# Kernel tuning notes

Hardware: AMD Instinct MI355X
Metric: run time of the kernel (lower is better)

The kernel has to match this reference:

```python
import jax, jax.numpy as jnp
import numpy as np

PAD = 1
VOCAB, D, HOPS = 32000, 256, 3

def _gru_dir(x_tbd, h0, Wih, Whh, bih, bhh):
    # x_tbd: [T,B,D]; PyTorch GRU gate math
    def step(h, xt):
        gx = xt @ Wih.T + bih            # [B,3D]
        gh = h @ Whh.T + bhh
        xr, xz, xn = jnp.split(gx, 3, axis=-1)
        hr, hz, hn = jnp.split(gh, 3, axis=-1)
        r = jax.nn.sigmoid(xr + hr)
        z = jax.nn.sigmoid(xz + hz)
        n = jnp.tanh(xn + r * hn)
        h2 = (1.0 - z) * n + z * h
        return h2, h2
    hT, ys = jax.lax.scan(step, h0, x_tbd)
    return ys, hT

def _embed_bag(table, idx):
    # idx: [B,L,M] -> sum over M -> [B,L,D]
    return jnp.take(table, idx, axis=0).sum(axis=2)

def _add_lm(full_mem, kb_len, conv_len, hiddens):
    # full_mem: [B,L,D]; hiddens: [B,T,D]; write hiddens into rows [kb, kb+cl)
    B, L, _ = full_mem.shape
    T = hiddens.shape[1]
    pos = jnp.arange(L)[None, :]                      # [1,L]
    rel = pos - kb_len[:, None]                        # [B,L]
    valid = (rel >= 0) & (rel < conv_len[:, None])
    rel_c = jnp.clip(rel, 0, T - 1)
    gathered = jnp.take_along_axis(hiddens, rel_c[:, :, None], axis=1)  # [B,L,D]
    return full_mem + jnp.where(valid[:, :, None], gathered, 0.0)

def setup_inputs() -> dict:
    key = jax.random.key(0)
    ks = jax.random.split(key, 20)
    B, T, L, M = 32, 128, 512, 4
    conv_seqs = jax.random.randint(ks[0], (B, T, M), 0, VOCAB)
    src_seqs = jax.random.randint(ks[1], (B, L, M), 0, VOCAB)
    kb_len = jnp.full((B,), L - T, dtype=jnp.int32)
    conv_len = jnp.full((B,), T, dtype=jnp.int32)
    def zero_pad(t):
        return t.at[PAD].set(0.0)
    emb_ctx = zero_pad(0.1 * jax.random.normal(ks[2], (VOCAB, D)))
    C_tables = zero_pad(0.1 * jax.random.normal(ks[3], (HOPS + 1, VOCAB, D)).transpose(1, 0, 2)).transpose(1, 0, 2)
    s = 1.0 / np.sqrt(D)
    Wih_f = jax.random.uniform(ks[4], (3 * D, D), minval=-s, maxval=s)
    Whh_f = jax.random.uniform(ks[5], (3 * D, D), minval=-s, maxval=s)
    bih_f = jax.random.uniform(ks[6], (3 * D,), minval=-s, maxval=s)
    bhh_f = jax.random.uniform(ks[7], (3 * D,), minval=-s, maxval=s)
    Wih_b = jax.random.uniform(ks[8], (3 * D, D), minval=-s, maxval=s)
    Whh_b = jax.random.uniform(ks[9], (3 * D, D), minval=-s, maxval=s)
    bih_b = jax.random.uniform(ks[10], (3 * D,), minval=-s, maxval=s)
    bhh_b = jax.random.uniform(ks[11], (3 * D,), minval=-s, maxval=s)
    W_w = jax.random.uniform(ks[12], (D, 2 * D), minval=-s, maxval=s)
    W_b = jax.random.uniform(ks[13], (D,), minval=-s, maxval=s)
    proj_w = jax.random.uniform(ks[14], (D, 2 * D), minval=-s, maxval=s)
    proj_b = jax.random.uniform(ks[15], (D,), minval=-s, maxval=s)
    return dict(conv_seqs=conv_seqs, src_seqs=src_seqs, kb_len=kb_len, conv_len=conv_len,
                emb_ctx=emb_ctx, C_tables=C_tables,
                Wih_f=Wih_f, Whh_f=Whh_f, bih_f=bih_f, bhh_f=bhh_f,
                Wih_b=Wih_b, Whh_b=Whh_b, bih_b=bih_b, bhh_b=bhh_b,
                W_w=W_w, W_b=W_b, proj_w=proj_w, proj_b=proj_b)

def reference(conv_seqs, src_seqs, kb_len, conv_len, emb_ctx, C_tables,
              Wih_f, Whh_f, bih_f, bhh_f, Wih_b, Whh_b, bih_b, bhh_b,
              W_w, W_b, proj_w, proj_b):
    B = conv_seqs.shape[0]
    # ContextRNN (dropout is identity at eval)
    emb = _embed_bag(emb_ctx, conv_seqs)               # [B,T,D]
    x = emb.transpose(1, 0, 2)                          # [T,B,D]
    h0 = jnp.zeros((B, D), emb.dtype)
    ys_f, hT_f = _gru_dir(x, h0, Wih_f, Whh_f, bih_f, bhh_f)
    ys_b, hT_b = _gru_dir(x[::-1], h0, Wih_b, Whh_b, bih_b, bhh_b)
    outputs = jnp.concatenate([ys_f, ys_b[::-1]], axis=-1).transpose(1, 0, 2)  # [B,T,2D]
    hidden = jnp.concatenate([hT_f, hT_b], axis=-1) @ W_w.T + W_b              # [B,D]
    rnn_out = outputs @ W_w.T + W_b                                            # [B,T,D]
    # ExternalKnowledge encode
    u = hidden
    prob_logit = None
    embed_C = None
    for hop in range(HOPS):
        embed_A = _add_lm(_embed_bag(C_tables[hop], src_seqs), kb_len, conv_len, rnn_out)
        embed_C = _add_lm(_embed_bag(C_tables[hop + 1], src_seqs), kb_len, conv_len, rnn_out)
        prob_logit = jnp.einsum('bld,bd->bl', embed_A, u)
        prob = jax.nn.softmax(prob_logit, axis=1)
        o_k = jnp.einsum('bld,bl->bd', embed_C, prob)
        u = u + o_k
    global_pointer = jax.nn.sigmoid(prob_logit)
    encoded = jax.nn.relu(jnp.concatenate([hidden, u], axis=-1) @ proj_w.T + proj_b)[None]
    return global_pointer, encoded
```

## Files before the change

kernel.cpp:

```cpp
#include <hip/hip_runtime.h>

typedef _Float16 f16;
typedef _Float16 f16x8 __attribute__((ext_vector_type(8)));
typedef _Float16 f16x4 __attribute__((ext_vector_type(4)));
typedef float    f32x4 __attribute__((ext_vector_type(4)));


__device__ __forceinline__ float frcp(float x){
  float r; asm("v_rcp_f32 %0, %1" : "=v"(r) : "v"(x)); return r;
}
__device__ __forceinline__ float fsig(float x){ return frcp(1.0f + __expf(-x)); }
__device__ __forceinline__ float ftanh(float x){ return 2.0f*frcp(1.0f + __expf(-2.0f*x)) - 1.0f; }

__global__ void k_zero(float* out){
  int i = blockIdx.x*256 + threadIdx.x;
  if (i < 24576) out[i] = 0.f;
}

__global__ __launch_bounds__(256) void k_prep(const float* __restrict__ s0,
                                              const float* __restrict__ s1,
                                              const float* __restrict__ s2,
                                              const float* __restrict__ s3,
                                              const float* __restrict__ s4,
                                              f16* __restrict__ d0, f16* __restrict__ d1,
                                              f16* __restrict__ d2, f16* __restrict__ d3,
                                              f16* __restrict__ d4,
                                              const int* __restrict__ conv,
                                              const float* __restrict__ tbl,
                                              f16* __restrict__ emb){
  int bid = blockIdx.x;
  if (bid < 768){
    int i = bid*256 + threadIdx.x;
    d0[i] = (f16)s0[i];
    d1[i] = (f16)s1[i];
    d2[i] = (f16)s2[i];
    d3[i] = (f16)s3[i];
    if (i < 131072) d4[i] = (f16)s4[i];
    return;
  }
  int bt = bid - 768, d = threadIdx.x;
  const int* ix = conv + (size_t)bt*4;
  float s = 0.f;
#pragma unroll
  for (int m = 0; m < 4; ++m) s += tbl[(size_t)ix[m]*256 + d];
  emb[(size_t)bt*256 + d] = (f16)s;
}

__global__ __launch_bounds__(256) void k_gx2(const f16* __restrict__ emb,
                                             const f16* __restrict__ wf,
                                             const f16* __restrict__ wb,
                                             const float* __restrict__ bih_f,
                                             const float* __restrict__ bhh_f,
                                             const float* __restrict__ bih_b,
                                             const float* __restrict__ bhh_b,
                                             f16* __restrict__ gx_f,
                                             f16* __restrict__ gx_b){
  int rev = blockIdx.x >> 6, blk = blockIdx.x & 63;
  const f16* W16 = rev ? wb : wf;
  const float* bih = rev ? bih_b : bih_f;
  const float* bhh = rev ? bhh_b : bhh_f;
  f16* gx = rev ? gx_b : gx_f;

  int lane = threadIdx.x & 63, wv = threadIdx.x >> 6;
  int l16 = lane & 15, l4 = lane >> 4;
  int mrow = blk*64 + wv*16;
  int m = mrow + l16;
  int t = m >> 5, b = m & 31;
  int tsrc = rev ? (127 - t) : t;
  const f16* arow = emb + (size_t)(b*128 + tsrc)*256;
  f16x8 af[8];
#pragma unroll
  for (int kt = 0; kt < 8; ++kt) af[kt] = *(const f16x8*)(arow + kt*32 + l4*8);

  for (int nt = 0; nt < 48; ++nt){
    int n = nt*16 + l16;
    const f16* brow = W16 + (size_t)n*256;
    f32x4 acc = {0.f,0.f,0.f,0.f};
#pragma unroll
    for (int kt = 0; kt < 8; ++kt){
      f16x8 bf = *(const f16x8*)(brow + kt*32 + l4*8);
      acc = __builtin_amdgcn_mfma_f32_16x16x32_f16(af[kt], bf, acc, 0, 0, 0);
    }
    float bias = bih[n] + (n < 512 ? bhh[n] : 0.f);
#pragma unroll
    for (int r = 0; r < 4; ++r){
      int m2 = mrow + l4*4 + r;
      gx[(size_t)m2*768 + n] = (f16)(acc[r] + bias);
    }
  }
}

__global__ __launch_bounds__(512, 1) void k_grumega(const f16* __restrict__ gx_f,
                                                    const f16* __restrict__ gx_b,
                                                    const f16* __restrict__ whhf16,
                                                    const f16* __restrict__ whhb16,
                                                    const float* __restrict__ bhh_f,
                                                    const float* __restrict__ bhh_b,
                                                    f16* __restrict__ Abuf,
                                                    const int* __restrict__ src,
                                                    const float* __restrict__ Ct,
                                                    f16* __restrict__ bagT,
                                                    int tab0, int tab1, int tab2, int tab3){
  int bid = blockIdx.x;
  if (bid >= 4){
    int gi = bid - 4;
    int slot = gi >> 6;
    int tab = slot == 0 ? tab0 : slot == 1 ? tab1 : slot == 2 ? tab2 : tab3;
    const float* tbl = Ct + (size_t)tab * 32000 * 256;
    f16* dst = bagT + (size_t)slot * 4194304;
    int tid = threadIdx.x;
    int d = tid & 255, half = tid >> 8;
    int base = (gi & 63) * 256;
#pragma unroll 2
    for (int it = 0; it < 128; ++it){
      int task = base + it*2 + half;
      int4 ix = *(const int4*)(src + (size_t)task*4);
      float s = tbl[(size_t)ix.x*256 + d] + tbl[(size_t)ix.y*256 + d]
              + tbl[(size_t)ix.z*256 + d] + tbl[(size_t)ix.w*256 + d];
      dst[(size_t)task*256 + d] = (f16)s;
    }
    return;
  }

  int dir = bid >> 1, grp = bid & 1, b0 = grp*16;
  const f16*   gx  = dir ? gx_b   : gx_f;
  const f16*   Whh = dir ? whhb16 : whhf16;
  const float* bhh = dir ? bhh_b  : bhh_f;

  int tid = threadIdx.x, lane = tid & 63, wv = tid >> 6;
  int l16 = lane & 15, l4 = lane >> 4;

  __shared__ __align__(16) f16   a16[2][16][264];
  __shared__ __align__(16) float bhnL[256];
  for (int i = tid; i < (16*264*2)/4; i += 512) ((unsigned*)&a16[0][0][0])[i] = 0u;
  if (tid < 256) bhnL[tid] = bhh[512 + tid];

  f16x8 aW[2][3][8];
#pragma unroll
  for (int q = 0; q < 2; ++q){
    int Q = 2*wv + q;
#pragma unroll
    for (int g = 0; g < 3; ++g){
      const f16* wrow = Whh + (size_t)(g*256 + Q*16 + l16)*256;
#pragma unroll
      for (int kt = 0; kt < 8; ++kt) aW[q][g][kt] = *(const f16x8*)(wrow + kt*32 + l4*8);
    }
  }

  const f16* gp = gx + (size_t)(b0 + l16)*768;
  f16* ap  = Abuf + (size_t)(b0 + l16)*128*512 + dir*256 + (size_t)(dir ? 127 : 0)*512;
  int  astep = dir ? -512 : 512;
  f16* app = ap;

  const int d00 = (2*wv    )*16 + l4*4;
  const int d01 = (2*wv + 1)*16 + l4*4;

  f16x4 pend[2];
  pend[0] = (f16x4){(f16)0.f,(f16)0.f,(f16)0.f,(f16)0.f};
  pend[1] = (f16x4){(f16)0.f,(f16)0.f,(f16)0.f,(f16)0.f};

  __syncthreads();

#pragma unroll 1
  for (int t = 0; t < 128; ++t){
    if (t){
      *(f16x4*)(app + d00) = pend[0];
      *(f16x4*)(app + d01) = pend[1];
    }
    f16x4 xg[2][3];
#pragma unroll
    for (int q = 0; q < 2; ++q)
#pragma unroll
      for (int g = 0; g < 3; ++g)
        xg[q][g] = *(const f16x4*)(gp + g*256 + (2*wv+q)*16 + l4*4);

    const f16* rb = &a16[t & 1][l16][l4*8];

    f32x4 accr[2], accz[2];
#pragma unroll
    for (int q = 0; q < 2; ++q){ accr[q] = (f32x4){0.f,0.f,0.f,0.f};
                                 accz[q] = (f32x4){0.f,0.f,0.f,0.f}; }
#pragma unroll
    for (int kt = 0; kt < 8; ++kt){
      f16x8 bf = *(const f16x8*)(rb + kt*32);
#pragma unroll
      for (int q = 0; q < 2; ++q){
        accr[q] = __builtin_amdgcn_mfma_f32_16x16x32_f16(aW[q][0][kt], bf, accr[q], 0, 0, 0);
        accz[q] = __builtin_amdgcn_mfma_f32_16x16x32_f16(aW[q][1][kt], bf, accz[q], 0, 0, 0);
      }
    }
    f32x4 accn[2];
#pragma unroll
    for (int q = 0; q < 2; ++q) accn[q] = (f32x4){0.f,0.f,0.f,0.f};
#pragma unroll
    for (int kt = 0; kt < 8; ++kt){
      f16x8 bf = *(const f16x8*)(rb + kt*32);
#pragma unroll
      for (int q = 0; q < 2; ++q)
        accn[q] = __builtin_amdgcn_mfma_f32_16x16x32_f16(aW[q][2][kt], bf, accn[q], 0, 0, 0);
    }
    float rr[2][4], zz[2][4];
#pragma unroll
    for (int q = 0; q < 2; ++q)
#pragma unroll
      for (int r = 0; r < 4; ++r){
        rr[q][r] = fsig((float)xg[q][0][r] + accr[q][r]);
        zz[q][r] = fsig((float)xg[q][1][r] + accz[q][r]);
      }
    int nxt = (t & 1) ^ 1;
#pragma unroll
    for (int q = 0; q < 2; ++q){
      int d0 = (2*wv+q)*16 + l4*4;
      float4 bh4 = *(const float4*)(&bhnL[d0]);
      f16x4 hold = pend[q];
      f16x4 o4;
#pragma unroll
      for (int r = 0; r < 4; ++r){
        float bh = (r==0)?bh4.x:(r==1)?bh4.y:(r==2)?bh4.z:bh4.w;
        float nn = ftanh((float)xg[q][2][r] + rr[q][r]*(accn[q][r] + bh));
        float h2 = nn + zz[q][r]*((float)hold[r] - nn);
        o4[r] = (f16)h2;
      }
      *(f16x4*)(&a16[nxt][l16][d0]) = o4;
      pend[q] = o4;
    }
    app = ap; ap += astep;
    gp += 24576;
    __syncthreads();
  }
  *(f16x4*)(app + d00) = pend[0];
  *(f16x4*)(app + d01) = pend[1];
}

__global__ __launch_bounds__(256) void k_post(const f16* __restrict__ Abuf,
                                              const f16* __restrict__ Ww16,
                                              const float* __restrict__ Wb,
                                              float* __restrict__ rnn,
                                              float* __restrict__ hidden,
                                              float* __restrict__ u){
  int bid = blockIdx.x;
  int lane = threadIdx.x & 63, wv = threadIdx.x >> 6;
  int l16 = lane & 15, l4 = lane >> 4;
  if (bid < 64){
    int mrow = bid*64 + wv*16;
    const f16* arow = Abuf + (size_t)(mrow + l16)*512;
    f16x8 af[16];
#pragma unroll
    for (int kt = 0; kt < 16; ++kt) af[kt] = *(const f16x8*)(arow + kt*32 + l4*8);
    for (int nt = 0; nt < 16; ++nt){
      int n = nt*16 + l16;
      const f16* brow = Ww16 + (size_t)n*512;
      f32x4 acc = {0.f,0.f,0.f,0.f};
#pragma unroll
      for (int kt = 0; kt < 16; ++kt){
        f16x8 bf = *(const f16x8*)(brow + kt*32 + l4*8);
        acc = __builtin_amdgcn_mfma_f32_16x16x32_f16(af[kt], bf, acc, 0, 0, 0);
      }
      float bias = Wb[n];
#pragma unroll
      for (int r = 0; r < 4; ++r)
        rnn[(size_t)(mrow + l4*4 + r)*256 + n] = acc[r] + bias;
    }
    return;
  }
  int hb = bid - 64;
  int mt = wv & 1, nt = hb*2 + (wv >> 1);
  int b = mt*16 + l16;
  const f16* rowf = Abuf + ((size_t)b*128 + 127)*512;
  const f16* rowb = Abuf + ((size_t)b*128)*512;
  f16x8 af[16];
#pragma unroll
  for (int kt = 0; kt < 16; ++kt){
    int k = kt*32 + l4*8;
    af[kt] = *(const f16x8*)((k < 256 ? rowf : rowb) + k);
  }
  int n = nt*16 + l16;
  const f16* brow = Ww16 + (size_t)n*512;
  f32x4 acc = {0.f,0.f,0.f,0.f};
#pragma unroll
  for (int kt = 0; kt < 16; ++kt){
    f16x8 bf = *(const f16x8*)(brow + kt*32 + l4*8);
    acc = __builtin_amdgcn_mfma_f32_16x16x32_f16(af[kt], bf, acc, 0, 0, 0);
  }
  float bias = Wb[n];
#pragma unroll
  for (int r = 0; r < 4; ++r){
    int bo = mt*16 + l4*4 + r;
    float v = acc[r] + bias;
    hidden[(size_t)bo*256 + n] = v;
    u[(size_t)bo*256 + n] = v;
  }
}

__global__ __launch_bounds__(256) void k_logits(const int* __restrict__ src,
                                                const int* __restrict__ kbl,
                                                const int* __restrict__ cvl,
                                                const float* __restrict__ tblA,
                                                const float* __restrict__ rnn,
                                                const float* __restrict__ u,
                                                float* __restrict__ logits,
                                                const f16* __restrict__ bag){
  int b = blockIdx.x >> 5, chunk = blockIdx.x & 31;
  int lane = threadIdx.x & 63, wv = threadIdx.x >> 6;
  int kb = kbl[b], cl = cvl[b];
  float4 uv = *(const float4*)(u + b*256 + lane*4);
#pragma unroll
  for (int i = 0; i < 4; ++i){
    int l = chunk*16 + wv*4 + i;
    float b0, b1, b2, b3;
    if (bag){
      f16x4 bv = *(const f16x4*)(bag + ((size_t)b*512 + l)*256 + lane*4);
      b0 = (float)bv[0]; b1 = (float)bv[1]; b2 = (float)bv[2]; b3 = (float)bv[3];
    } else {
      const int* sp = src + ((size_t)b*512 + l)*4;
      b0 = b1 = b2 = b3 = 0.f;
#pragma unroll
      for (int m = 0; m < 4; ++m){
        float4 wq = *(const float4*)(tblA + (size_t)sp[m]*256 + lane*4);
        b0 += wq.x; b1 += wq.y; b2 += wq.z; b3 += wq.w;
      }
    }
    int rel = l - kb;
    if (rel >= 0 && rel < cl){
      int rc = rel < 127 ? rel : 127;
      float4 rv = *(const float4*)(rnn + ((size_t)b*128 + rc)*256 + lane*4);
      b0 += rv.x; b1 += rv.y; b2 += rv.z; b3 += rv.w;
    }
    float p = b0*uv.x + b1*uv.y + b2*uv.z + b3*uv.w;
#pragma unroll
    for (int off = 32; off >= 1; off >>= 1) p += __shfl_down(p, off);
    if (lane == 0) logits[(size_t)b*512 + l] = p;
  }
}

__global__ __launch_bounds__(256) void k_okv(const int* __restrict__ src,
                                             const int* __restrict__ kbl,
                                             const int* __restrict__ cvl,
                                             const float* __restrict__ tblC,
                                             const float* __restrict__ rnn,
                                             const float* __restrict__ logits,
                                             float* __restrict__ u,
                                             float* __restrict__ gp_out, int write_gp,
                                             const f16* __restrict__ bagin,
                                             f16* __restrict__ bagout){
  int b = blockIdx.x >> 4, c = blockIdx.x & 15;
  int d = threadIdx.x, lane = d & 63, wv = d >> 6;
  __shared__ float red[4];
  __shared__ float bc;
  __shared__ float pr[512];
  __shared__ int   sidx[128];

  float v0 = logits[(size_t)b*512 + d];
  float v1 = logits[(size_t)b*512 + 256 + d];
  float m = fmaxf(v0, v1);
#pragma unroll
  for (int off = 32; off >= 1; off >>= 1) m = fmaxf(m, __shfl_down(m, off));
  if (lane == 0) red[wv] = m;
  __syncthreads();
  if (d == 0) bc = fmaxf(fmaxf(red[0], red[1]), fmaxf(red[2], red[3]));
  __syncthreads();
  float mx = bc;
  float e0 = __expf(v0 - mx), e1 = __expf(v1 - mx);
  float s = e0 + e1;
#pragma unroll
  for (int off = 32; off >= 1; off >>= 1) s += __shfl_down(s, off);
  __syncthreads();
  if (lane == 0) red[wv] = s;
  __syncthreads();
  if (d == 0) bc = red[0] + red[1] + red[2] + red[3];
  __syncthreads();
  float inv = 1.0f/bc;
  pr[d] = e0*inv; pr[256 + d] = e1*inv;
  if (d < 128) sidx[d] = src[(size_t)b*2048 + c*128 + d];
  if (write_gp && c == 0){
    gp_out[(size_t)b*512 + d]       = fsig(v0);
    gp_out[(size_t)b*512 + 256 + d] = fsig(v1);
  }
  __syncthreads();

  int kb = kbl[b], cl = cvl[b];
  float acc = 0.f;
  for (int l = 0; l < 32; ++l){
    float bag;
    if (bagin){
      bag = (float)bagin[((size_t)b*512 + c*32 + l)*256 + d];
    } else {
      const int* sp = sidx + l*4;
      bag = tblC[(size_t)sp[0]*256 + d] + tblC[(size_t)sp[1]*256 + d]
          + tblC[(size_t)sp[2]*256 + d] + tblC[(size_t)sp[3]*256 + d];
      if (bagout) bagout[((size_t)b*512 + c*32 + l)*256 + d] = (f16)bag;
    }
    int rel = (c*32 + l) - kb;
    if (rel >= 0 && rel < cl){
      int rc = rel < 127 ? rel : 127;
      bag += rnn[((size_t)b*128 + rc)*256 + d];
    }
    acc += pr[c*32 + l] * bag;
  }
  atomicAdd(&u[(size_t)b*256 + d], acc);
}

__global__ void k_encoded(const float* __restrict__ hidden, const float* __restrict__ u,
                          const float* __restrict__ pw, const float* __restrict__ pb,
                          float* __restrict__ out){
  int b = blockIdx.x, d = threadIdx.x;
  const float* w = pw + (size_t)d*512;
  float s = pb[d];
  for (int k = 0; k < 256; ++k) s += hidden[b*256 + k] * w[k];
  for (int k = 0; k < 256; ++k) s += u[b*256 + k]      * w[256 + k];
  out[(size_t)b*256 + d] = fmaxf(s, 0.f);
}

extern "C" void kernel_launch(void* const* d_in, const int* in_sizes, int n_in,
                              void* d_out, int out_size, void* d_ws, size_t ws_size,
                              hipStream_t stream){
  (void)in_sizes; (void)n_in; (void)out_size;
  float* out = (float*)d_out;

  const size_t WS_NEEDED = 25034752;
  if (ws_size < WS_NEEDED){
    k_zero<<<96, 256, 0, stream>>>(out);
    return;
  }

  const int* conv  = (const int*)d_in[0];
  const int* src   = (const int*)d_in[1];
  const int* kbl   = (const int*)d_in[2];
  const int* cvl   = (const int*)d_in[3];
  const float* emb_ctx = (const float*)d_in[4];
  const float* Ct      = (const float*)d_in[5];
  const float* Wih_f = (const float*)d_in[6];
  const float* Whh_f = (const float*)d_in[7];
  const float* bih_f = (const float*)d_in[8];
  const float* bhh_f = (const float*)d_in[9];
  const float* Wih_b = (const float*)d_in[10];
  const float* Whh_b = (const float*)d_in[11];
  const float* bih_b = (const float*)d_in[12];
  const float* bhh_b = (const float*)d_in[13];
  const float* Ww = (const float*)d_in[14];
  const float* Wb = (const float*)d_in[15];
  const float* pw = (const float*)d_in[16];
  const float* pb = (const float*)d_in[17];

  char* ws = (char*)d_ws;
  f16*   emb    = (f16*)(ws);
  f16*   gx_f   = (f16*)(ws + 2097152);
  f16*   gx_b   = (f16*)(ws + 8388608);
  f16*   Abuf   = (f16*)(ws + 14680064);
  float* rnn    = (float*)(ws + 18874368);
  float* hidden = (float*)(ws + 23068672);
  float* u      = (float*)(ws + 23101440);
  float* logits = (float*)(ws + 23134208);
  f16*   wihf16 = (f16*)(ws + 23199744);
  f16*   wihb16 = (f16*)(ws + 23592960);
  f16*   whhf16 = (f16*)(ws + 23986176);
  f16*   whhb16 = (f16*)(ws + 24379392);
  f16*   ww16   = (f16*)(ws + 24772608);
  f16*   bagbuf = (f16*)(ws + 2097152);
  f16*   bagT   = (f16*)(ws + WS_NEEDED);
  size_t avail  = ws_size - WS_NEEDED;
  int ntab = (int)(avail / 8388608); if (ntab > 4) ntab = 4;
  const int tabids[4] = {1, 2, 3, 0};
  const f16* bt[4] = {nullptr, nullptr, nullptr, nullptr};
  for (int s = 0; s < ntab; ++s) bt[tabids[s]] = bagT + (size_t)s*4194304;

  k_prep<<<4864, 256, 0, stream>>>(Wih_f, Wih_b, Whh_f, Whh_b, Ww,
                                   wihf16, wihb16, whhf16, whhb16, ww16,
                                   conv, emb_ctx, emb);
  k_gx2<<<128, 256, 0, stream>>>(emb, wihf16, wihb16,
                                 bih_f, bhh_f, bih_b, bhh_b, gx_f, gx_b);
  k_grumega<<<4 + 64*ntab, 512, 0, stream>>>(gx_f, gx_b, whhf16, whhb16,
                                             bhh_f, bhh_b, Abuf,
                                             src, Ct, bagT,
                                             tabids[0], tabids[1], tabids[2], tabids[3]);
  k_post<<<72, 256, 0, stream>>>(Abuf, ww16, Wb, rnn, hidden, u);

  for (int hop = 0; hop < 3; ++hop){
    const float* tA = Ct + (size_t)hop     * 32000 * 256;
    const float* tC = Ct + (size_t)(hop+1) * 32000 * 256;
    const f16* lbag = bt[hop] ? bt[hop] : (hop ? bagbuf : (const f16*)nullptr);
    const f16* obag = bt[hop + 1];
    f16* obout = (!obag && hop < 2) ? bagbuf : (f16*)nullptr;
    k_logits<<<1024, 256, 0, stream>>>(src, kbl, cvl, tA, rnn, u, logits, lbag);
    k_okv<<<512, 256, 0, stream>>>(src, kbl, cvl, tC, rnn, logits, u,
                                   out, hop == 2 ? 1 : 0, obag, obout);
  }
  k_encoded<<<32, 256, 0, stream>>>(hidden, u, pw, pb, out + 16384);
}
```

Measured before the change: 745.3 us.

## Fuse each memory hop into one per-batch kernel when all bags are precomputed

When all four embedding-bag tables are precomputed in workspace, each hop's logits, softmax, weighted sum and u update run in a single 32-block kernel per hop. The last hop also computes the global pointer and the encoded projection, which replaces the separate logits, okv and encoded launches. This removes launch overhead and intermediate logits traffic. The cost is only 32 blocks of parallelism, with per-thread serial 256-element loops, including strided column reads over the C bag.

```diff
diff --git a/kernel.cpp b/kernel.cpp
--- a/kernel.cpp
+++ b/kernel.cpp
@@ -292,6 +292,120 @@
   }
 }
 
+__global__ __launch_bounds__(512) void k_hop(const int* __restrict__ kbl,
+                                             const int* __restrict__ cvl,
+                                             const f16* __restrict__ bagA,
+                                             const f16* __restrict__ bagC,
+                                             const float* __restrict__ rnn,
+                                             float* __restrict__ u,
+                                             float* __restrict__ gp_out, int last,
+                                             const float* __restrict__ hidden,
+                                             const float* __restrict__ pw,
+                                             const float* __restrict__ pb,
+                                             float* __restrict__ enc_out){
+  int b = blockIdx.x, tid = threadIdx.x;
+  int lane = tid & 63, wvi = tid >> 6;
+  __shared__ float uL[256];
+  __shared__ float pr[512];
+  __shared__ float redm[8], reds[8];
+  __shared__ float bcast;
+  __shared__ float part[2][256];
+
+  if (tid < 256) uL[tid] = u[(size_t)b*256 + tid];
+  __syncthreads();
+
+  int kb = kbl[b], cl = cvl[b];
+
+  const f16* brow = bagA + ((size_t)b*512 + tid)*256;
+  int rel = tid - kb;
+  bool inr = (rel >= 0 && rel < cl);
+  int rc = rel < 127 ? rel : 127;
+  const float* rrow = rnn + ((size_t)b*128 + (inr ? rc : 0))*256;
+  float dot = 0.f;
+  if (inr){
+    for (int k = 0; k < 256; k += 8){
+      f16x8 bv = *(const f16x8*)(brow + k);
+      float4 r0 = *(const float4*)(rrow + k);
+      float4 r1 = *(const float4*)(rrow + k + 4);
+      dot += ((float)bv[0]+r0.x)*uL[k+0] + ((float)bv[1]+r0.y)*uL[k+1]
+           + ((float)bv[2]+r0.z)*uL[k+2] + ((float)bv[3]+r0.w)*uL[k+3]
+           + ((float)bv[4]+r1.x)*uL[k+4] + ((float)bv[5]+r1.y)*uL[k+5]
+           + ((float)bv[6]+r1.z)*uL[k+6] + ((float)bv[7]+r1.w)*uL[k+7];
+    }
+  } else {
+    for (int k = 0; k < 256; k += 8){
+      f16x8 bv = *(const f16x8*)(brow + k);
+      dot += (float)bv[0]*uL[k+0] + (float)bv[1]*uL[k+1]
+           + (float)bv[2]*uL[k+2] + (float)bv[3]*uL[k+3]
+           + (float)bv[4]*uL[k+4] + (float)bv[5]*uL[k+5]
+           + (float)bv[6]*uL[k+6] + (float)bv[7]*uL[k+7];
+    }
+  }
+  if (last) gp_out[(size_t)b*512 + tid] = fsig(dot);
+
+  float m = dot;
+#pragma unroll
+  for (int off = 32; off >= 1; off >>= 1) m = fmaxf(m, __shfl_down(m, off));
+  if (lane == 0) redm[wvi] = m;
+  __syncthreads();
+  if (tid == 0){
+    float mm = redm[0];
+#pragma unroll
+    for (int i = 1; i < 8; ++i) mm = fmaxf(mm, redm[i]);
+    bcast = mm;
+  }
+  __syncthreads();
+  float e = __expf(dot - bcast);
+  float s = e;
+#pragma unroll
+  for (int off = 32; off >= 1; off >>= 1) s += __shfl_down(s, off);
+  if (lane == 0) reds[wvi] = s;
+  __syncthreads();
+  float stot = reds[0]+reds[1]+reds[2]+reds[3]+reds[4]+reds[5]+reds[6]+reds[7];
+  pr[tid] = e * frcp(stot);
+  __syncthreads();
+
+  int d = tid & 255, hf = tid >> 8;
+  const f16* cbase = bagC + ((size_t)b*512 + hf*256)*256 + d;
+  const float* rbase = rnn + (size_t)b*128*256 + d;
+  float acc = 0.f;
+  for (int l = 0; l < 256; ++l){
+    int gl = hf*256 + l;
+    float bag = (float)cbase[(size_t)l*256];
+    int r2 = gl - kb;
+    if (r2 >= 0 && r2 < cl){
+      int rc2 = r2 < 127 ? r2 : 127;
+      bag += rbase[(size_t)rc2*256];
+    }
+    acc += pr[gl] * bag;
+  }
+  part[hf][d] = acc;
+  __syncthreads();
+  if (tid < 256){
+    float un = uL[tid] + part[0][tid] + part[1][tid];
+    u[(size_t)b*256 + tid] = un;
+    uL[tid] = un;
+  }
+  __syncthreads();
+
+  if (last){
+    __shared__ float hL[256];
+    if (tid < 256) hL[tid] = hidden[(size_t)b*256 + tid];
+    __syncthreads();
+    const float* w = pw + (size_t)d*512 + hf*256;
+    const float* xv = hf ? uL : hL;
+    float sacc = 0.f;
+    for (int k = 0; k < 256; k += 4){
+      float4 wq = *(const float4*)(w + k);
+      sacc += wq.x*xv[k] + wq.y*xv[k+1] + wq.z*xv[k+2] + wq.w*xv[k+3];
+    }
+    part[hf][d] = sacc;
+    __syncthreads();
+    if (tid < 256)
+      enc_out[(size_t)b*256 + tid] = fmaxf(part[0][tid] + part[1][tid] + pb[tid], 0.f);
+  }
+}
+
 __global__ __launch_bounds__(256) void k_logits(const int* __restrict__ src,
                                                 const int* __restrict__ kbl,
                                                 const int* __restrict__ cvl,
@@ -475,15 +589,22 @@
                                              tabids[0], tabids[1], tabids[2], tabids[3]);
   k_post<<<72, 256, 0, stream>>>(Abuf, ww16, Wb, rnn, hidden, u);
 
-  for (int hop = 0; hop < 3; ++hop){
-    const float* tA = Ct + (size_t)hop     * 32000 * 256;
-    const float* tC = Ct + (size_t)(hop+1) * 32000 * 256;
-    const f16* lbag = bt[hop] ? bt[hop] : (hop ? bagbuf : (const f16*)nullptr);
-    const f16* obag = bt[hop + 1];
-    f16* obout = (!obag && hop < 2) ? bagbuf : (f16*)nullptr;
-    k_logits<<<1024, 256, 0, stream>>>(src, kbl, cvl, tA, rnn, u, logits, lbag);
-    k_okv<<<512, 256, 0, stream>>>(src, kbl, cvl, tC, rnn, logits, u,
-                                   out, hop == 2 ? 1 : 0, obag, obout);
-  }
-  k_encoded<<<32, 256, 0, stream>>>(hidden, u, pw, pb, out + 16384);
-}
+  if (ntab == 4){
+    for (int hop = 0; hop < 3; ++hop)
+      k_hop<<<32, 512, 0, stream>>>(kbl, cvl, bt[hop], bt[hop+1], rnn, u,
+                                    out, hop == 2 ? 1 : 0,
+                                    hidden, pw, pb, out + 16384);
+  } else {
+    for (int hop = 0; hop < 3; ++hop){
+      const float* tA = Ct + (size_t)hop     * 32000 * 256;
+      const float* tC = Ct + (size_t)(hop+1) * 32000 * 256;
+      const f16* lbag = bt[hop] ? bt[hop] : (hop ? bagbuf : (const f16*)nullptr);
+      const f16* obag = bt[hop + 1];
+      f16* obout = (!obag && hop < 2) ? bagbuf : (f16*)nullptr;
+      k_logits<<<1024, 256, 0, stream>>>(src, kbl, cvl, tA, rnn, u, logits, lbag);
+      k_okv<<<512, 256, 0, stream>>>(src, kbl, cvl, tC, rnn, logits, u,
+                                     out, hop == 2 ? 1 : 0, obag, obout);
+    }
+    k_encoded<<<32, 256, 0, stream>>>(hidden, u, pw, pb, out + 16384);
+  }
+}
```

Measured after the change: 1.004 ms. 1.35x slower.

## Fuse memory-network hop into single kernel and inline embedding gather into gx GEMM

Applied to the files above, without the earlier changes.

When all four bag tables fit in the workspace, each hop's logits, softmax and weighted sum over C now run in one kernel per hop (128 blocks), accumulating o_k with atomics, instead of separate logits and okv kernels. This removes a launch and a round trip of logits through global memory per hop. The context embedding-bag sum moves from k_prep into k_gx2, where it is staged in LDS, and output zeroing folds into k_post as an extra block. The risks are the small 128-block grid per hop and float atomics making the result order-dependent.

```diff
diff --git a/kernel.cpp b/kernel.cpp
--- a/kernel.cpp
+++ b/kernel.cpp
@@ -24,29 +24,17 @@
                                               const float* __restrict__ s4,
                                               f16* __restrict__ d0, f16* __restrict__ d1,
                                               f16* __restrict__ d2, f16* __restrict__ d3,
-                                              f16* __restrict__ d4,
-                                              const int* __restrict__ conv,
-                                              const float* __restrict__ tbl,
-                                              f16* __restrict__ emb){
-  int bid = blockIdx.x;
-  if (bid < 768){
-    int i = bid*256 + threadIdx.x;
-    d0[i] = (f16)s0[i];
-    d1[i] = (f16)s1[i];
-    d2[i] = (f16)s2[i];
-    d3[i] = (f16)s3[i];
-    if (i < 131072) d4[i] = (f16)s4[i];
-    return;
-  }
-  int bt = bid - 768, d = threadIdx.x;
-  const int* ix = conv + (size_t)bt*4;
-  float s = 0.f;
-#pragma unroll
-  for (int m = 0; m < 4; ++m) s += tbl[(size_t)ix[m]*256 + d];
-  emb[(size_t)bt*256 + d] = (f16)s;
-}
-
-__global__ __launch_bounds__(256) void k_gx2(const f16* __restrict__ emb,
+                                              f16* __restrict__ d4){
+  int i = blockIdx.x*256 + threadIdx.x;
+  d0[i] = (f16)s0[i];
+  d1[i] = (f16)s1[i];
+  d2[i] = (f16)s2[i];
+  d3[i] = (f16)s3[i];
+  if (i < 131072) d4[i] = (f16)s4[i];
+}
+
+__global__ __launch_bounds__(256) void k_gx2(const int* __restrict__ conv,
+                                             const float* __restrict__ etbl,
                                              const f16* __restrict__ wf,
                                              const f16* __restrict__ wb,
                                              const float* __restrict__ bih_f,
@@ -61,13 +49,24 @@
   const float* bhh = rev ? bhh_b : bhh_f;
   f16* gx = rev ? gx_b : gx_f;
 
-  int lane = threadIdx.x & 63, wv = threadIdx.x >> 6;
+  int tid = threadIdx.x;
+  int lane = tid & 63, wv = tid >> 6;
   int l16 = lane & 15, l4 = lane >> 4;
+
+  __shared__ __align__(16) f16 embL[64][264];
+  for (int r = 0; r < 64; ++r){
+    int m = blk*64 + r;
+    int t = m >> 5, b = m & 31;
+    int tsrc = rev ? (127 - t) : t;
+    const int* ix = conv + (size_t)(b*128 + tsrc)*4;
+    float s = etbl[(size_t)ix[0]*256 + tid] + etbl[(size_t)ix[1]*256 + tid]
+            + etbl[(size_t)ix[2]*256 + tid] + etbl[(size_t)ix[3]*256 + tid];
+    embL[r][tid] = (f16)s;
+  }
+  __syncthreads();
+
   int mrow = blk*64 + wv*16;
-  int m = mrow + l16;
-  int t = m >> 5, b = m & 31;
-  int tsrc = rev ? (127 - t) : t;
-  const f16* arow = emb + (size_t)(b*128 + tsrc)*256;
+  const f16* arow = &embL[wv*16 + l16][0];
   f16x8 af[8];
 #pragma unroll
   for (int kt = 0; kt < 8; ++kt) af[kt] = *(const f16x8*)(arow + kt*32 + l4*8);
@@ -237,10 +236,15 @@
                                               const float* __restrict__ Wb,
                                               float* __restrict__ rnn,
                                               float* __restrict__ hidden,
-                                              float* __restrict__ u){
+                                              float* __restrict__ u,
+                                              float* __restrict__ ozero){
   int bid = blockIdx.x;
   int lane = threadIdx.x & 63, wv = threadIdx.x >> 6;
   int l16 = lane & 15, l4 = lane >> 4;
+  if (bid == 72){
+    for (int i = threadIdx.x; i < 24576; i += 256) ozero[i] = 0.f;
+    return;
+  }
   if (bid < 64){
     int mrow = bid*64 + wv*16;
     const f16* arow = Abuf + (size_t)(mrow + l16)*512;
@@ -290,6 +294,115 @@
     hidden[(size_t)bo*256 + n] = v;
     u[(size_t)bo*256 + n] = v;
   }
+}
+
+__global__ __launch_bounds__(512) void k_hop2(const int* __restrict__ kbl,
+                                              const int* __restrict__ cvl,
+                                              const f16* __restrict__ bagA,
+                                              const f16* __restrict__ bagC,
+                                              const float* __restrict__ rnn,
+                                              const float* __restrict__ u0,
+                                              float* __restrict__ o0,
+                                              float* __restrict__ o1,
+                                              float* __restrict__ o2,
+                                              int hop,
+                                              float* __restrict__ gp_out){
+  int b = blockIdx.x >> 2, c = blockIdx.x & 3;
+  int tid = threadIdx.x, lane = tid & 63, wvi = tid >> 6;
+  __shared__ float uL[256];
+  __shared__ float lgL[512];
+  __shared__ float prL[512];
+  __shared__ float redm[8], reds[8];
+  __shared__ float bcast;
+  __shared__ float part[2][256];
+
+  if (tid < 256){
+    float v = u0[(size_t)b*256 + tid];
+    if (hop >= 1) v += o0[(size_t)b*256 + tid];
+    if (hop >= 2) v += o1[(size_t)b*256 + tid];
+    uL[tid] = v;
+  }
+  __syncthreads();
+
+  int kb = kbl[b], cl = cvl[b];
+  float4 uv = *(const float4*)(&uL[lane*4]);
+
+  for (int i = 0; i < 64; ++i){
+    int l = wvi*64 + i;
+    f16x4 bv = *(const f16x4*)(bagA + ((size_t)b*512 + l)*256 + lane*4);
+    float p0 = (float)bv[0], p1 = (float)bv[1], p2 = (float)bv[2], p3 = (float)bv[3];
+    int rel = l - kb;
+    if (rel >= 0 && rel < cl){
+      int rc = rel < 127 ? rel : 127;
+      float4 rv = *(const float4*)(rnn + ((size_t)b*128 + rc)*256 + lane*4);
+      p0 += rv.x; p1 += rv.y; p2 += rv.z; p3 += rv.w;
+    }
+    float p = p0*uv.x + p1*uv.y + p2*uv.z + p3*uv.w;
+#pragma unroll
+    for (int off = 32; off >= 1; off >>= 1) p += __shfl_down(p, off);
+    if (lane == 0) lgL[l] = p;
+  }
+  __syncthreads();
+
+  if (hop == 2 && c == 0) gp_out[(size_t)b*512 + tid] = fsig(lgL[tid]);
+
+  float v = lgL[tid];
+  float m = v;
+#pragma unroll
+  for (int off = 32; off >= 1; off >>= 1) m = fmaxf(m, __shfl_down(m, off));
+  if (lane == 0) redm[wvi] = m;
+  __syncthreads();
+  if (tid == 0){
+    float mm = redm[0];
+#pragma unroll
+    for (int i = 1; i < 8; ++i) mm = fmaxf(mm, redm[i]);
+    bcast = mm;
+  }
+  __syncthreads();
+  float e = __expf(v - bcast);
+  float s = e;
+#pragma unroll
+  for (int off = 32; off >= 1; off >>= 1) s += __shfl_down(s, off);
+  if (lane == 0) reds[wvi] = s;
+  __syncthreads();
+  float stot = reds[0]+reds[1]+reds[2]+reds[3]+reds[4]+reds[5]+reds[6]+reds[7];
+  prL[tid] = e * frcp(stot);
+  __syncthreads();
+
+  int d = tid & 255, hf = tid >> 8;
+  float acc = 0.f;
+  for (int i = 0; i < 64; ++i){
+    int gl = c*128 + hf*64 + i;
+    float bag = (float)bagC[((size_t)b*512 + gl)*256 + d];
+    int rel = gl - kb;
+    if (rel >= 0 && rel < cl){
+      int rc = rel < 127 ? rel : 127;
+      bag += rnn[((size_t)b*128 + rc)*256 + d];
+    }
+    acc += prL[gl] * bag;
+  }
+  part[hf][d] = acc;
+  __syncthreads();
+  float* oT = hop == 0 ? o0 : hop == 1 ? o1 : o2;
+  if (tid < 256) atomicAdd(&oT[(size_t)b*256 + tid], part[0][tid] + part[1][tid]);
+}
+
+__global__ void k_encoded2(const float* __restrict__ hidden, const float* __restrict__ u0,
+                           const float* __restrict__ o0, const float* __restrict__ o1,
+                           const float* __restrict__ o2,
+                           const float* __restrict__ pw, const float* __restrict__ pb,
+                           float* __restrict__ out){
+  int b = blockIdx.x, d = threadIdx.x;
+  __shared__ float hL[256], uf[256];
+  hL[d] = hidden[(size_t)b*256 + d];
+  uf[d] = u0[(size_t)b*256 + d] + o0[(size_t)b*256 + d]
+        + o1[(size_t)b*256 + d] + o2[(size_t)b*256 + d];
+  __syncthreads();
+  const float* w = pw + (size_t)d*512;
+  float s = pb[d];
+  for (int k = 0; k < 256; ++k) s += hL[k] * w[k];
+  for (int k = 0; k < 256; ++k) s += uf[k] * w[256 + k];
+  out[(size_t)b*256 + d] = fmaxf(s, 0.f);
 }
 
 __global__ __launch_bounds__(256) void k_logits(const int* __restrict__ src,
@@ -443,7 +556,9 @@
   const float* pb = (const float*)d_in[17];
 
   char* ws = (char*)d_ws;
-  f16*   emb    = (f16*)(ws);
+  float* o0    = (float*)(ws);
+  float* o1    = (float*)(ws + 32768);
+  float* o2    = (float*)(ws + 65536);
   f16*   gx_f   = (f16*)(ws + 2097152);
   f16*   gx_b   = (f16*)(ws + 8388608);
   f16*   Abuf   = (f16*)(ws + 14680064);
@@ -464,26 +579,32 @@
   const f16* bt[4] = {nullptr, nullptr, nullptr, nullptr};
   for (int s = 0; s < ntab; ++s) bt[tabids[s]] = bagT + (size_t)s*4194304;
 
-  k_prep<<<4864, 256, 0, stream>>>(Wih_f, Wih_b, Whh_f, Whh_b, Ww,
-                                   wihf16, wihb16, whhf16, whhb16, ww16,
-                                   conv, emb_ctx, emb);
-  k_gx2<<<128, 256, 0, stream>>>(emb, wihf16, wihb16,
+  k_prep<<<768, 256, 0, stream>>>(Wih_f, Wih_b, Whh_f, Whh_b, Ww,
+                                  wihf16, wihb16, whhf16, whhb16, ww16);
+  k_gx2<<<128, 256, 0, stream>>>(conv, emb_ctx, wihf16, wihb16,
                                  bih_f, bhh_f, bih_b, bhh_b, gx_f, gx_b);
   k_grumega<<<4 + 64*ntab, 512, 0, stream>>>(gx_f, gx_b, whhf16, whhb16,
                                              bhh_f, bhh_b, Abuf,
                                              src, Ct, bagT,
                                              tabids[0], tabids[1], tabids[2], tabids[3]);
-  k_post<<<72, 256, 0, stream>>>(Abuf, ww16, Wb, rnn, hidden, u);
-
-  for (int hop = 0; hop < 3; ++hop){
-    const float* tA = Ct + (size_t)hop     * 32000 * 256;
-    const float* tC = Ct + (size_t)(hop+1) * 32000 * 256;
-    const f16* lbag = bt[hop] ? bt[hop] : (hop ? bagbuf : (const f16*)nullptr);
-    const f16* obag = bt[hop + 1];
-    f16* obout = (!obag && hop < 2) ? bagbuf : (f16*)nullptr;
-    k_logits<<<1024, 256, 0, stream>>>(src, kbl, cvl, tA, rnn, u, logits, lbag);
-    k_okv<<<512, 256, 0, stream>>>(src, kbl, cvl, tC, rnn, logits, u,
-                                   out, hop == 2 ? 1 : 0, obag, obout);
-  }
-  k_encoded<<<32, 256, 0, stream>>>(hidden, u, pw, pb, out + 16384);
-}
+  k_post<<<73, 256, 0, stream>>>(Abuf, ww16, Wb, rnn, hidden, u, o0);
+
+  if (ntab == 4){
+    for (int hop = 0; hop < 3; ++hop)
+      k_hop2<<<128, 512, 0, stream>>>(kbl, cvl, bt[hop], bt[hop+1], rnn,
+                                      u, o0, o1, o2, hop, out);
+    k_encoded2<<<32, 256, 0, stream>>>(hidden, u, o0, o1, o2, pw, pb, out + 16384);
+  } else {
+    for (int hop = 0; hop < 3; ++hop){
+      const float* tA = Ct + (size_t)hop     * 32000 * 256;
+      const float* tC = Ct + (size_t)(hop+1) * 32000 * 256;
+      const f16* lbag = bt[hop] ? bt[hop] : (hop ? bagbuf : (const f16*)nullptr);
+      const f16* obag = bt[hop + 1];
+      f16* obout = (!obag && hop < 2) ? bagbuf : (f16*)nullptr;
+      k_logits<<<1024, 256, 0, stream>>>(src, kbl, cvl, tA, rnn, u, logits, lbag);
+      k_okv<<<512, 256, 0, stream>>>(src, kbl, cvl, tC, rnn, logits, u,
+                                     out, hop == 2 ? 1 : 0, obag, obout);
+    }
+    k_encoded<<<32, 256, 0, stream>>>(hidden, u, pw, pb, out + 16384);
+  }
+}
```

Result: slower. 912.0 us (+22.4%).
